# Kernel tuning notes

Hardware: AMD Instinct MI355X
Metric: run time of the kernel (lower is better)

## Reference

```python
import jax, jax.numpy as jnp
import numpy as np


def setup_inputs() -> dict:
    key = jax.random.key(0)
    k1, k2, k3 = jax.random.split(key, 3)
    E = 2_000_000   # number of events (messages)
    N = 1_000_000   # number of nodes
    D = 128         # message feature dim
    node_ids = jax.random.randint(k1, (E,), 0, N, dtype=jnp.int32)
    msg = jax.random.normal(k2, (E, D), dtype=jnp.float32)
    times = jax.random.uniform(k3, (E,), dtype=jnp.float32)
    return {"node_ids": node_ids, "msg": msg, "times": times, "num_nodes": N}


def reference(node_ids, msg, times, num_nodes):
    # Last event index per node (segment 'last' == segment_max over event index).
    E = node_ids.shape[0]
    ev_idx = jnp.arange(E, dtype=jnp.int32)
    last_idx = jax.ops.segment_max(ev_idx, node_ids, num_segments=num_nodes)
    # Nodes with no messages get INT32_MIN from segment_max -> invalid.
    valid = last_idx >= 0                      # [N] bool, stands in for to_update_node_ids
    safe_idx = jnp.where(valid, last_idx, 0)   # clamp for gather
    unique_msg = jnp.where(valid[:, None], msg[safe_idx], 0.0)   # [N, D]
    unique_times = jnp.where(valid, times[safe_idx], 0.0)        # [N]
    return valid, unique_msg, unique_times
```

## Files before the change

kernel.cpp:

```cpp
#include <hip/hip_runtime.h>
#include <hip/hip_bf16.h>

typedef float vf4 __attribute__((ext_vector_type(4)));

__global__ void k_init_last(int4* __restrict__ last_idx4, int n4) {
    int stride = gridDim.x * blockDim.x;
    for (int i = blockIdx.x * blockDim.x + threadIdx.x; i < n4; i += stride) {
        last_idx4[i] = make_int4(-1, -1, -1, -1);
    }
}

__global__ void k_last_idx(const int* __restrict__ node_ids,
                           int* __restrict__ last_idx, int E) {
    int i = blockIdx.x * blockDim.x + threadIdx.x;
    if (i < E) {
        atomicMax(&last_idx[node_ids[i]], i);
    }
}

__global__ void k_gather(const vf4* __restrict__ msg,
                         const int* __restrict__ last_idx,
                         const float* __restrict__ times,
                         vf4* __restrict__ out_msg,
                         float* __restrict__ out_valid,
                         float* __restrict__ out_times, int N) {
    int t = blockIdx.x * blockDim.x + threadIdx.x;
    int node = t >> 3;
    int q = t & 7;
    if (node >= N) return;
    int li = last_idx[node];
    size_t obase = (size_t)node * 32 + q;
    if (li >= 0) {
        size_t ibase = (size_t)li * 32 + q;
        vf4 v0 = __builtin_nontemporal_load(&msg[ibase]);
        vf4 v1 = __builtin_nontemporal_load(&msg[ibase + 8]);
        vf4 v2 = __builtin_nontemporal_load(&msg[ibase + 16]);
        vf4 v3 = __builtin_nontemporal_load(&msg[ibase + 24]);
        __builtin_nontemporal_store(v0, &out_msg[obase]);
        __builtin_nontemporal_store(v1, &out_msg[obase + 8]);
        __builtin_nontemporal_store(v2, &out_msg[obase + 16]);
        __builtin_nontemporal_store(v3, &out_msg[obase + 24]);
    } else {
        vf4 z = (vf4)0.0f;
        __builtin_nontemporal_store(z, &out_msg[obase]);
        __builtin_nontemporal_store(z, &out_msg[obase + 8]);
        __builtin_nontemporal_store(z, &out_msg[obase + 16]);
        __builtin_nontemporal_store(z, &out_msg[obase + 24]);
    }
    if (q == 0) {
        out_valid[node] = (li >= 0) ? 1.0f : 0.0f;
        out_times[node] = (li >= 0) ? times[li] : 0.0f;
    }
}

extern "C" void kernel_launch(void* const* d_in, const int* in_sizes, int n_in,
                              void* d_out, int out_size, void* d_ws, size_t ws_size,
                              hipStream_t stream) {
    const int*   node_ids = (const int*)d_in[0];
    const float* msg      = (const float*)d_in[1];
    const float* times    = (const float*)d_in[2];
    const int E = in_sizes[0];
    const int N = out_size / 130;

    float* out_valid = (float*)d_out;
    float* out_msg   = (float*)d_out + N;
    float* out_times = (float*)d_out + N + (size_t)N * 128;

    int* last_idx = (int*)d_ws;

    const int B = 256;

    int n4 = N / 4;
    k_init_last<<<2048, B, 0, stream>>>((int4*)last_idx, n4);

    k_last_idx<<<(E + B - 1) / B, B, 0, stream>>>(node_ids, last_idx, E);

    long long total = (long long)N * 8;
    k_gather<<<(int)((total + B - 1) / B), B, 0, stream>>>(
        (const vf4*)msg, last_idx, times,
        (vf4*)out_msg, out_valid, out_times, N);
}
```

Measured before the change: 251.5 us.

## Replace node-side gather with event-side scatter plus zero-fill pass

Switches from gathering each node's last message to scattering from events whose index equals the node's last index, so message reads become sequential. A second kernel zero-fills rows, validity and times for nodes with no events. This adds a second pass over node_ids, random lookups of last_idx per event, launches far more threads, and makes output writes random.

```diff
diff --git a/kernel.cpp b/kernel.cpp
--- a/kernel.cpp
+++ b/kernel.cpp
@@ -18,9 +18,37 @@
     }
 }
 
-__global__ void k_gather(const vf4* __restrict__ msg,
-                         const int* __restrict__ last_idx,
-                         const float* __restrict__ times,
+__global__ void k_scatter(const vf4* __restrict__ msg,
+                          const int* __restrict__ node_ids,
+                          const int* __restrict__ last_idx,
+                          const float* __restrict__ times,
+                          vf4* __restrict__ out_msg,
+                          float* __restrict__ out_valid,
+                          float* __restrict__ out_times, int E) {
+    int t = blockIdx.x * blockDim.x + threadIdx.x;
+    int ev = t >> 3;
+    int q = t & 7;
+    if (ev >= E) return;
+    int nid = node_ids[ev];
+    int li = last_idx[nid];
+    if (li != ev) return;
+    size_t ib = (size_t)ev * 32 + q;
+    size_t ob = (size_t)nid * 32 + q;
+    vf4 v0 = __builtin_nontemporal_load(&msg[ib]);
+    vf4 v1 = __builtin_nontemporal_load(&msg[ib + 8]);
+    vf4 v2 = __builtin_nontemporal_load(&msg[ib + 16]);
+    vf4 v3 = __builtin_nontemporal_load(&msg[ib + 24]);
+    __builtin_nontemporal_store(v0, &out_msg[ob]);
+    __builtin_nontemporal_store(v1, &out_msg[ob + 8]);
+    __builtin_nontemporal_store(v2, &out_msg[ob + 16]);
+    __builtin_nontemporal_store(v3, &out_msg[ob + 24]);
+    if (q == 0) {
+        out_valid[nid] = 1.0f;
+        out_times[nid] = times[ev];
+    }
+}
+
+__global__ void k_finish(const int* __restrict__ last_idx,
                          vf4* __restrict__ out_msg,
                          float* __restrict__ out_valid,
                          float* __restrict__ out_times, int N) {
@@ -29,27 +57,16 @@
     int q = t & 7;
     if (node >= N) return;
     int li = last_idx[node];
-    size_t obase = (size_t)node * 32 + q;
-    if (li >= 0) {
-        size_t ibase = (size_t)li * 32 + q;
-        vf4 v0 = __builtin_nontemporal_load(&msg[ibase]);
-        vf4 v1 = __builtin_nontemporal_load(&msg[ibase + 8]);
-        vf4 v2 = __builtin_nontemporal_load(&msg[ibase + 16]);
-        vf4 v3 = __builtin_nontemporal_load(&msg[ibase + 24]);
-        __builtin_nontemporal_store(v0, &out_msg[obase]);
-        __builtin_nontemporal_store(v1, &out_msg[obase + 8]);
-        __builtin_nontemporal_store(v2, &out_msg[obase + 16]);
-        __builtin_nontemporal_store(v3, &out_msg[obase + 24]);
-    } else {
-        vf4 z = (vf4)0.0f;
-        __builtin_nontemporal_store(z, &out_msg[obase]);
-        __builtin_nontemporal_store(z, &out_msg[obase + 8]);
-        __builtin_nontemporal_store(z, &out_msg[obase + 16]);
-        __builtin_nontemporal_store(z, &out_msg[obase + 24]);
-    }
+    if (li >= 0) return;
+    size_t ob = (size_t)node * 32 + q;
+    vf4 z = (vf4)0.0f;
+    __builtin_nontemporal_store(z, &out_msg[ob]);
+    __builtin_nontemporal_store(z, &out_msg[ob + 8]);
+    __builtin_nontemporal_store(z, &out_msg[ob + 16]);
+    __builtin_nontemporal_store(z, &out_msg[ob + 24]);
     if (q == 0) {
-        out_valid[node] = (li >= 0) ? 1.0f : 0.0f;
-        out_times[node] = (li >= 0) ? times[li] : 0.0f;
+        out_valid[node] = 0.0f;
+        out_times[node] = 0.0f;
     }
 }
 
@@ -70,13 +87,16 @@
 
     const int B = 256;
 
-    int n4 = N / 4;
-    k_init_last<<<2048, B, 0, stream>>>((int4*)last_idx, n4);
+    k_init_last<<<2048, B, 0, stream>>>((int4*)last_idx, N / 4);
 
     k_last_idx<<<(E + B - 1) / B, B, 0, stream>>>(node_ids, last_idx, E);
 
-    long long total = (long long)N * 8;
-    k_gather<<<(int)((total + B - 1) / B), B, 0, stream>>>(
-        (const vf4*)msg, last_idx, times,
-        (vf4*)out_msg, out_valid, out_times, N);
+    long long ts = (long long)E * 8;
+    k_scatter<<<(int)((ts + B - 1) / B), B, 0, stream>>>(
+        (const vf4*)msg, node_ids, last_idx, times,
+        (vf4*)out_msg, out_valid, out_times, E);
+
+    long long tf = (long long)N * 8;
+    k_finish<<<(int)((tf + B - 1) / B), B, 0, stream>>>(
+        last_idx, (vf4*)out_msg, out_valid, out_times, N);
 }
```

After: 295.9 us. 1.18x slower.
